# Performance work log

Measured on AMD Instinct MI355X. Metric: run time of the kernel, lower is better.

## Reference

```python
import jax, jax.numpy as jnp
import numpy as np

N, IN_DIM, D = 8192, 1024, 512


def setup_inputs() -> dict:
    key = jax.random.key(0)
    ks = jax.random.split(key, 11)
    s_in = 1.0 / np.sqrt(IN_DIM)
    s_d = 1.0 / np.sqrt(D)
    s_h = 1.0 / np.sqrt(D // 2)
    return {
        "x": jax.random.normal(ks[0], (N, IN_DIM), jnp.float32),
        # torch Linear weights stored as [in, out] for x @ W + b
        "Wq": jax.random.uniform(ks[1], (IN_DIM, D), jnp.float32, -s_in, s_in),
        "bq": jax.random.uniform(ks[2], (D,), jnp.float32, -s_in, s_in),
        "Wk": jax.random.uniform(ks[3], (IN_DIM, D), jnp.float32, -s_in, s_in),
        "bk": jax.random.uniform(ks[4], (D,), jnp.float32, -s_in, s_in),
        "Wv": jax.random.uniform(ks[5], (IN_DIM, D), jnp.float32, -s_in, s_in),
        "bv": jax.random.uniform(ks[6], (D,), jnp.float32, -s_in, s_in),
        "W1": jax.random.uniform(ks[7], (D, D // 2), jnp.float32, -s_d, s_d),
        "b1": jax.random.uniform(ks[8], (D // 2,), jnp.float32, -s_d, s_d),
        "W2": jax.random.uniform(ks[9], (D // 2, 1), jnp.float32, -s_h, s_h),
        "b2": jax.random.uniform(ks[10], (1,), jnp.float32, -s_h, s_h),
    }


def reference(x, Wq, bq, Wk, bk, Wv, bv, W1, b1, W2, b2):
    d = Wq.shape[1]
    q = x @ Wq + bq            # [N, D]
    k = x @ Wk + bk            # [N, D]
    v = x @ Wv + bv            # [N, D]
    attn = jax.nn.softmax((q @ k.T) / jnp.sqrt(jnp.float32(d)), axis=-1)  # [N, N]
    # original does sum_j attn[i,j] * v[j]  ==  attn @ v (no O(N^2 D) intermediate)
    ctx = attn @ v             # [N, D]
    h = jax.nn.relu(ctx @ W1 + b1)   # [N, D/2]
    scores = (h @ W2 + b2).squeeze(-1)  # [N]
    return scores
```

## Files before the change

### kernel.cpp

```cpp
#include <hip/hip_runtime.h>
#include <hip/hip_bf16.h>
#include <cstdint>
#include <cstddef>

typedef float  f32x4  __attribute__((ext_vector_type(4)));
typedef __bf16 bf16x8 __attribute__((ext_vector_type(8)));
typedef __bf16 bf16x4 __attribute__((ext_vector_type(4)));

#define N_TOK  8192
#define INDIM  1024
#define DMODEL 512
#define NHALF  4096

__device__ __forceinline__ f32x4 mfma16x16x32(bf16x8 a, bf16x8 b, f32x4 c){
  return __builtin_amdgcn_mfma_f32_16x16x32_bf16(a, b, c, 0, 0, 0);
}

__device__ __forceinline__ void async_copy16(void* lds, const void* g){
  __builtin_amdgcn_global_load_lds((__attribute__((address_space(1))) void*)g,
                                   (__attribute__((address_space(3))) void*)lds,
                                   16, 0, 0);
}

__global__ void k_cvt(const float* __restrict__ in, __bf16* __restrict__ out, int n4){
  int stride = gridDim.x * blockDim.x;
  for (int i = blockIdx.x * blockDim.x + threadIdx.x; i < n4; i += stride){
    f32x4 v = ((const f32x4*)in)[i];
    bf16x4 o;
    o[0]=(__bf16)v[0]; o[1]=(__bf16)v[1]; o[2]=(__bf16)v[2]; o[3]=(__bf16)v[3];
    ((bf16x4*)out)[i] = o;
  }
}

__global__ void k_tcvt(const float* __restrict__ W, __bf16* __restrict__ Wt, int Kd, int Nd){
  int total = Kd * Nd;
  int stride = gridDim.x * blockDim.x;
  for (int i = blockIdx.x * blockDim.x + threadIdx.x; i < total; i += stride){
    int k = i / Nd, n = i - k * Nd;
    Wt[(size_t)n * Kd + k] = (__bf16)W[i];
  }
}

__global__ void k_bias2(const float* __restrict__ a, const float* __restrict__ b,
                        float* __restrict__ o){
  int idx = blockIdx.x * 256 + threadIdx.x;
  o[idx] = (idx < 512) ? a[idx] : b[idx - 512];
}

template<int EPI, int MAP, int RSUM>
__global__ __launch_bounds__(256) void k_gemm(
    const __bf16* __restrict__ A, const __bf16* __restrict__ Bt,
    const float* __restrict__ bias, __bf16* __restrict__ C,
    int M, int N, int K, int lda, int ldb, int ldc, float scale,
    float* __restrict__ rsp, int rbase)
{
  __shared__ __bf16 Als[2][128][32];
  __shared__ __bf16 Bls[2][128][32];
  const int tid = threadIdx.x;
  const int w = tid >> 6, l = tid & 63;
  const int lr = l & 15, lg = l >> 4;
  const int wr = w >> 1, wc = w & 1;
  int m0, n0, kz, zsel;
  if (MAP == 0){
    m0 = blockIdx.x * 128; n0 = blockIdx.y * 128; zsel = blockIdx.z; kz = zsel * K;
  } else if (MAP == 1){
    int lin = blockIdx.x, xcd = lin & 7, idx = lin >> 3;
    m0 = (xcd*8 + (idx & 7)) * 128; n0 = (idx >> 3) * 128; zsel = 0; kz = 0;
  } else {
    int lin = blockIdx.x, xcd = lin & 7, i = lin >> 3;
    zsel = xcd >> 2; kz = zsel * K;
    m0 = ((xcd & 3)*16 + (i >> 2)) * 128; n0 = (i & 3) * 128;
  }
  const int srow = l >> 2;
  const int skof = (l & 3) * 8;

  auto stage = [&](int b, int kk){
    #pragma unroll
    for (int i = 0; i < 2; ++i){
      int c = i * 4 + w;
      async_copy16((char*)&Als[b][0][0] + c * 1024,
                   A  + (size_t)(m0 + c*16 + srow) * lda + kk + skof);
      async_copy16((char*)&Bls[b][0][0] + c * 1024,
                   Bt + (size_t)(n0 + c*16 + srow) * ldb + kk + skof);
    }
  };

  f32x4 acc[4][4] = {};
  const int nt = K >> 5;
  stage(0, kz);
  __syncthreads();
  for (int t = 0; t < nt; ++t){
    const int cur = t & 1;
    if (t + 1 < nt) stage(cur ^ 1, kz + (t+1)*32);
    bf16x8 af[4], bfv[4];
    #pragma unroll
    for (int mf = 0; mf < 4; ++mf) af[mf]  = *(const bf16x8*)&Als[cur][wr*64 + mf*16 + lr][lg*8];
    #pragma unroll
    for (int nf = 0; nf < 4; ++nf) bfv[nf] = *(const bf16x8*)&Bls[cur][wc*64 + nf*16 + lr][lg*8];
    #pragma unroll
    for (int mf = 0; mf < 4; ++mf)
      #pragma unroll
      for (int nf = 0; nf < 4; ++nf)
        acc[mf][nf] = mfma16x16x32(af[mf], bfv[nf], acc[mf][nf]);
    __syncthreads();
  }
  __bf16* Cd = C + (size_t)zsel * (size_t)M * ldc;
  float rsp4[4][4];
  #pragma unroll
  for (int mf = 0; mf < 4; ++mf)
    #pragma unroll
    for (int r = 0; r < 4; ++r) rsp4[mf][r] = 0.0f;
  #pragma unroll
  for (int mf = 0; mf < 4; ++mf)
    #pragma unroll
    for (int nf = 0; nf < 4; ++nf)
      #pragma unroll
      for (int r = 0; r < 4; ++r){
        int row = m0 + wr*64 + mf*16 + lg*4 + r;
        int col = n0 + wc*64 + nf*16 + lr;
        float v = acc[mf][nf][r];
        if (EPI == 0) v += bias[col];
        if (EPI == 2) v = __expf(v * scale);
        Cd[(size_t)row * ldc + col] = (__bf16)v;
        if (RSUM) rsp4[mf][r] += v;
      }
  if (RSUM){
    #pragma unroll
    for (int mf = 0; mf < 4; ++mf)
      #pragma unroll
      for (int r = 0; r < 4; ++r)
        #pragma unroll
        for (int dl = 1; dl < 16; dl <<= 1)
          rsp4[mf][r] += __shfl_xor(rsp4[mf][r], dl);
    if (lr == 0){
      int cb = rbase + (n0 >> 6) + wc;
      #pragma unroll
      for (int mf = 0; mf < 4; ++mf)
        #pragma unroll
        for (int r = 0; r < 4; ++r)
          rsp[(size_t)cb * N_TOK + m0 + wr*64 + mf*16 + lg*4 + r] = rsp4[mf][r];
    }
  }
}

__global__ __launch_bounds__(256) void k_rsum(
    const float* __restrict__ rsp, float* __restrict__ rs)
{
  int row = blockIdx.x * 256 + threadIdx.x;
  float s = 0.0f;
  #pragma unroll 8
  for (int j = 0; j < 128; ++j) s += rsp[(size_t)j * N_TOK + row];
  rs[row] = s;
}

__global__ __launch_bounds__(256) void k_vcomb(
    const __bf16* __restrict__ p, const float* __restrict__ bv,
    __bf16* __restrict__ vtb)
{
  int idx = blockIdx.x * 256 + threadIdx.x;
  int row = idx >> 10;
  float b = bv[row];
  bf16x8 a = ((const bf16x8*)p)[idx];
  bf16x8 c = ((const bf16x8*)(p + (size_t)DMODEL * N_TOK))[idx];
  bf16x8 o;
  #pragma unroll
  for (int i = 0; i < 8; ++i)
    o[i] = (__bf16)((float)a[i] + (float)c[i] + b);
  ((bf16x8*)vtb)[idx] = o;
}

__global__ __launch_bounds__(256) void k_mlp(
    const __bf16* __restrict__ p00, const __bf16* __restrict__ p01,
    const __bf16* __restrict__ p10, const __bf16* __restrict__ p11,
    const float* __restrict__ rs, const __bf16* __restrict__ W1t,
    const float* __restrict__ b1, const float* __restrict__ W2,
    const float* __restrict__ b2, float* __restrict__ out)
{
  __shared__ __bf16 Als[64][512];
  __shared__ float  red[4][64];
  const int tid = threadIdx.x;
  const int w = tid >> 6, l = tid & 63;
  const int lr = l & 15, lg = l >> 4;
  const int m0 = blockIdx.x * 64;
  #pragma unroll
  for (int i = 0; i < 16; ++i){
    int chunk = i*256 + tid;
    int rl = chunk >> 6, c8 = chunk & 63;
    size_t off = (size_t)(m0 + rl) * 64 + c8;
    float inv = 1.0f / rs[m0 + rl];
    bf16x8 a = ((const bf16x8*)p00)[off];
    bf16x8 b = ((const bf16x8*)p01)[off];
    bf16x8 c = ((const bf16x8*)p10)[off];
    bf16x8 d = ((const bf16x8*)p11)[off];
    bf16x8 o;
    #pragma unroll
    for (int j = 0; j < 8; ++j)
      o[j] = (__bf16)((((float)a[j] + (float)b[j]) + ((float)c[j] + (float)d[j])) * inv);
    *(bf16x8*)&Als[rl][c8*8] = o;
  }
  __syncthreads();
  f32x4 acc[4][4] = {};
  for (int t = 0; t < 16; ++t){
    bf16x8 af[4];
    #pragma unroll
    for (int mf2 = 0; mf2 < 4; ++mf2) af[mf2] = *(const bf16x8*)&Als[mf2*16 + lr][t*32 + lg*8];
    #pragma unroll
    for (int nf2 = 0; nf2 < 4; ++nf2){
      bf16x8 bfr = *(const bf16x8*)&W1t[(size_t)(w*64 + nf2*16 + lr)*DMODEL + t*32 + lg*8];
      #pragma unroll
      for (int mf2 = 0; mf2 < 4; ++mf2)
        acc[mf2][nf2] = mfma16x16x32(af[mf2], bfr, acc[mf2][nf2]);
    }
  }
  float part[4][4] = {};
  #pragma unroll
  for (int nf2 = 0; nf2 < 4; ++nf2){
    int col = w*64 + nf2*16 + lr;
    float bb = b1[col], w2v = W2[col];
    #pragma unroll
    for (int mf2 = 0; mf2 < 4; ++mf2)
      #pragma unroll
      for (int r = 0; r < 4; ++r){
        float h = acc[mf2][nf2][r] + bb;
        h = h > 0.0f ? h : 0.0f;
        part[mf2][r] += h * w2v;
      }
  }
  #pragma unroll
  for (int mf2 = 0; mf2 < 4; ++mf2)
    #pragma unroll
    for (int r = 0; r < 4; ++r)
      #pragma unroll
      for (int dl = 1; dl < 16; dl <<= 1)
        part[mf2][r] += __shfl_xor(part[mf2][r], dl);
  if (lr == 0){
    #pragma unroll
    for (int mf2 = 0; mf2 < 4; ++mf2)
      #pragma unroll
      for (int r = 0; r < 4; ++r)
        red[w][mf2*16 + lg*4 + r] = part[mf2][r];
  }
  __syncthreads();
  if (tid < 64)
    out[m0 + tid] = red[0][tid] + red[1][tid] + red[2][tid] + red[3][tid] + b2[0];
}

extern "C" void kernel_launch(void* const* d_in, const int* in_sizes, int n_in,
                              void* d_out, int out_size, void* d_ws, size_t ws_size,
                              hipStream_t stream)
{
  const float* x  = (const float*)d_in[0];
  const float* Wq = (const float*)d_in[1];
  const float* bq = (const float*)d_in[2];
  const float* Wk = (const float*)d_in[3];
  const float* bk = (const float*)d_in[4];
  const float* Wv = (const float*)d_in[5];
  const float* bv = (const float*)d_in[6];
  const float* W1 = (const float*)d_in[7];
  const float* b1 = (const float*)d_in[8];
  const float* W2 = (const float*)d_in[9];
  const float* b2 = (const float*)d_in[10];
  float* out = (float*)d_out;
  char* ws = (char*)d_ws;
  __bf16* xb   = (__bf16*)(ws + 0);
  __bf16* qkb  = (__bf16*)(ws + 16777216);
  __bf16* vtb  = (__bf16*)(ws + 33554432);
  __bf16* wqkt = (__bf16*)(ws + 50331648);
  __bf16* wvt  = (__bf16*)(ws + 52428800);
  __bf16* w1t  = (__bf16*)(ws + 53477376);
  float*  rs   = (float*)(ws + 53739520);
  float*  bqk  = (float*)(ws + 53772288);
  float*  rsp  = (float*)(ws + 54525952);
  __bf16* Ph   = (__bf16*)(ws + 58720256);
  __bf16* vpp  = (__bf16*)(ws + 58720256);
  __bf16* p00  = (__bf16*)(ws + 0);
  __bf16* p01  = (__bf16*)(ws + 8388608);
  __bf16* p10  = (__bf16*)(ws + 16777216);
  __bf16* p11  = (__bf16*)(ws + 25165824);

  k_cvt<<<2048, 256, 0, stream>>>(x, xb, N_TOK*INDIM/4);
  k_tcvt<<<512, 256, 0, stream>>>(Wq, wqkt, INDIM, DMODEL);
  k_tcvt<<<512, 256, 0, stream>>>(Wk, wqkt + (size_t)DMODEL*INDIM, INDIM, DMODEL);
  k_tcvt<<<512, 256, 0, stream>>>(Wv, wvt, INDIM, DMODEL);
  k_tcvt<<<256, 256, 0, stream>>>(W1, w1t, DMODEL, DMODEL/2);
  k_bias2<<<4, 256, 0, stream>>>(bq, bk, bqk);

  k_gemm<0,0,0><<<dim3(64, 8), 256, 0, stream>>>(xb, wqkt, bqk, qkb,
      N_TOK, 2*DMODEL, INDIM, INDIM, INDIM, 2*DMODEL, 0.f, nullptr, 0);
  k_gemm<3,0,0><<<dim3(4, 64, 2), 256, 0, stream>>>(wvt, xb, nullptr, vpp,
      DMODEL, N_TOK, INDIM/2, INDIM, INDIM, N_TOK, 0.f, nullptr, 0);
  k_vcomb<<<DMODEL*N_TOK/8/256, 256, 0, stream>>>(vpp, bv, vtb);

  const float scale = 0.04419417382415922f;
  const __bf16* Qm = qkb;
  const __bf16* Km = qkb + DMODEL;
  k_gemm<2,1,1><<<2048, 256, 0, stream>>>(Qm, Km, nullptr, Ph,
      N_TOK, NHALF, DMODEL, 2*DMODEL, 2*DMODEL, NHALF, scale, rsp, 0);
  k_gemm<3,2,0><<<512, 256, 0, stream>>>(Ph, vtb, nullptr, p00,
      N_TOK, DMODEL, NHALF/2, NHALF, N_TOK, DMODEL, 0.f, nullptr, 0);
  k_gemm<2,1,1><<<2048, 256, 0, stream>>>(Qm, Km + (size_t)NHALF*2*DMODEL, nullptr, Ph,
      N_TOK, NHALF, DMODEL, 2*DMODEL, 2*DMODEL, NHALF, scale, rsp, 64);
  k_gemm<3,2,0><<<512, 256, 0, stream>>>(Ph, vtb + NHALF, nullptr, p10,
      N_TOK, DMODEL, NHALF/2, NHALF, N_TOK, DMODEL, 0.f, nullptr, 0);

  k_rsum<<<32, 256, 0, stream>>>(rsp, rs);
  k_mlp<<<N_TOK/64, 256, 0, stream>>>(p00, p01, p10, p11, rs,
      w1t, b1, W2, b2, out);

  (void)in_sizes; (void)n_in; (void)out_size; (void)ws_size;
}
```

Before: 298.2 us.

## Double GEMM K-tile to 64 with XOR-swizzled LDS layout

Raises the GEMM K step per LDS stage from 32 to 64, which halves the number of barrier and stage iterations. The tile is stored in LDS as 128x64 rows with an XOR swizzle on 16-byte chunks to avoid bank conflicts on the fragment reads. Shared memory use doubles to 64KB per block, which may lower occupancy. K must now be a multiple of 64.

```diff
diff --git a/kernel.cpp b/kernel.cpp
--- a/kernel.cpp
+++ b/kernel.cpp
@@ -54,8 +54,8 @@
     int M, int N, int K, int lda, int ldb, int ldc, float scale,
     float* __restrict__ rsp, int rbase)
 {
-  __shared__ __bf16 Als[2][128][32];
-  __shared__ __bf16 Bls[2][128][32];
+  __shared__ __bf16 Als[2][128*64];
+  __shared__ __bf16 Bls[2][128*64];
   const int tid = threadIdx.x;
   const int w = tid >> 6, l = tid & 63;
   const int lr = l & 15, lg = l >> 4;
@@ -71,37 +71,44 @@
     zsel = xcd >> 2; kz = zsel * K;
     m0 = ((xcd & 3)*16 + (i >> 2)) * 128; n0 = (i & 3) * 128;
   }
-  const int srow = l >> 2;
-  const int skof = (l & 3) * 8;
+  const int srow = w*8 + (l >> 3);
+  const int scol = ((l & 7) ^ (l >> 3)) * 8;
 
   auto stage = [&](int b, int kk){
     #pragma unroll
-    for (int i = 0; i < 2; ++i){
-      int c = i * 4 + w;
-      async_copy16((char*)&Als[b][0][0] + c * 1024,
-                   A  + (size_t)(m0 + c*16 + srow) * lda + kk + skof);
-      async_copy16((char*)&Bls[b][0][0] + c * 1024,
-                   Bt + (size_t)(n0 + c*16 + srow) * ldb + kk + skof);
-    }
+    for (int ro = 0; ro < 4; ++ro)
+      async_copy16((char*)&Als[b][0] + ro*4096 + w*1024,
+                   A  + (size_t)(m0 + ro*32 + srow) * lda + kk + scol);
+    #pragma unroll
+    for (int ro = 0; ro < 4; ++ro)
+      async_copy16((char*)&Bls[b][0] + ro*4096 + w*1024,
+                   Bt + (size_t)(n0 + ro*32 + srow) * ldb + kk + scol);
   };
 
   f32x4 acc[4][4] = {};
-  const int nt = K >> 5;
+  const int nt = K >> 6;
   stage(0, kz);
   __syncthreads();
+  const int r7 = lr & 7;
   for (int t = 0; t < nt; ++t){
     const int cur = t & 1;
-    if (t + 1 < nt) stage(cur ^ 1, kz + (t+1)*32);
-    bf16x8 af[4], bfv[4];
-    #pragma unroll
-    for (int mf = 0; mf < 4; ++mf) af[mf]  = *(const bf16x8*)&Als[cur][wr*64 + mf*16 + lr][lg*8];
-    #pragma unroll
-    for (int nf = 0; nf < 4; ++nf) bfv[nf] = *(const bf16x8*)&Bls[cur][wc*64 + nf*16 + lr][lg*8];
-    #pragma unroll
-    for (int mf = 0; mf < 4; ++mf)
+    if (t + 1 < nt) stage(cur ^ 1, kz + (t+1)*64);
+    #pragma unroll
+    for (int kk = 0; kk < 2; ++kk){
+      const int cs = ((kk*4 + lg) ^ r7) * 8;
+      bf16x8 af[4], bfv[4];
+      #pragma unroll
+      for (int mf = 0; mf < 4; ++mf)
+        af[mf]  = *(const bf16x8*)&Als[cur][(wr*64 + mf*16 + lr)*64 + cs];
       #pragma unroll
       for (int nf = 0; nf < 4; ++nf)
-        acc[mf][nf] = mfma16x16x32(af[mf], bfv[nf], acc[mf][nf]);
+        bfv[nf] = *(const bf16x8*)&Bls[cur][(wc*64 + nf*16 + lr)*64 + cs];
+      #pragma unroll
+      for (int mf = 0; mf < 4; ++mf)
+        #pragma unroll
+        for (int nf = 0; nf < 4; ++nf)
+          acc[mf][nf] = mfma16x16x32(af[mf], bfv[nf], acc[mf][nf]);
+    }
     __syncthreads();
   }
   __bf16* Cd = C + (size_t)zsel * (size_t)M * ldc;
```

Result: faster. 271.5 us (median of 2 runs) (-8.9%).
